# Kernel optimization log

Measured on AMD Instinct MI355X. Metric: run time of the kernel, lower is better.

## Reference

```python
import jax, jax.numpy as jnp
import numpy as np

B, T, D = 8, 1024, 1024
H = 16
DH = D // H  # 64


def setup_inputs() -> dict:
    key = jax.random.key(0)
    k1, k2, k3 = jax.random.split(key, 3)
    x = jax.random.normal(k1, (B, T, D), dtype=jnp.float32)
    W_qkv = jax.random.normal(k2, (3 * D, D), dtype=jnp.float32) * (D ** -0.5)
    W_proj = jax.random.normal(k3, (D, D), dtype=jnp.float32) * (D ** -0.5)
    return {"x": x, "W_qkv": W_qkv, "W_proj": W_proj}


def reference(x, W_qkv, W_proj):
    b, t, _ = x.shape
    # qkv: [B,T,3*D] -> [B,T,3,H,DH]
    qkv = (x @ W_qkv.T).reshape(b, t, 3, H, DH)
    q, k, v = qkv[:, :, 0], qkv[:, :, 1], qkv[:, :, 2]  # [B,T,H,DH]
    scale = DH ** -0.5
    # scores: [B,H,Tq,Tk]
    scores = jnp.einsum("bqhd,bkhd->bhqk", q, k) * scale
    # NOTE: softmax over dim=-2 (the QUERY axis), as in the original module
    attn = jax.nn.softmax(scores, axis=-2)
    out = jnp.einsum("bhqk,bkhd->bqhd", attn, v).reshape(b, t, D)
    return out @ W_proj.T
```

## Files before the change

### kernel.cpp

```cpp
#include <hip/hip_runtime.h>


typedef __bf16 bf16_t;
typedef __bf16 bf16x8 __attribute__((ext_vector_type(8)));
typedef __bf16 bf16x4 __attribute__((ext_vector_type(4)));
typedef float f32x4 __attribute__((ext_vector_type(4)));
typedef unsigned short u16x8 __attribute__((ext_vector_type(8)));

#define DEV __device__ __forceinline__
#define C2 0.18033688f

DEV void gld_lds16(const bf16_t* g, bf16_t* l) {
  __builtin_amdgcn_global_load_lds(
      (const __attribute__((address_space(1))) unsigned int*)g,
      (__attribute__((address_space(3))) unsigned int*)l, 16, 0, 0);
}

DEV float exp2c(float x) { return __builtin_amdgcn_exp2f(fminf(x, 30.f)); }
DEV float sanit(float v) { return (v == v) ? fminf(fmaxf(v, -1e4f), 1e4f) : 0.f; }

DEV int sw64(int r, int kc) { return r * 64 + (((kc ^ (r + (r >> 3))) & 7) << 3); }

DEV f32x4 mfma16(bf16x8 a, bf16x8 b, f32x4 c) {
  return __builtin_amdgcn_mfma_f32_16x16x32_bf16(a, b, c, 0, 0, 0);
}

__global__ void detect_dtype(const unsigned short* x, int* flag) {
  __shared__ int smax;
  if (threadIdx.x == 0) smax = 0;
  __syncthreads();
  int m = 0;
  for (int i = threadIdx.x; i < 16384; i += 256) {
    int e = (x[i] >> 7) & 0xFF;
    m = m > e ? m : e;
  }
  atomicMax(&smax, m);
  __syncthreads();
  if (threadIdx.x == 0) *flag = (smax >= 160) ? 1 : 0;
}

__global__ void convert_in(const void* __restrict__ x, const void* __restrict__ wq,
                           const void* __restrict__ wp, bf16_t* __restrict__ xb,
                           bf16_t* __restrict__ wqb, bf16_t* __restrict__ wpb,
                           const int* __restrict__ flag) {
  int i = blockIdx.x * 256 + threadIdx.x;
  const void* src;
  bf16_t* dst;
  int off;
  if (i < 1048576) { src = x; dst = xb; off = i; }
  else if (i < 1441792) { src = wq; dst = wqb; off = i - 1048576; }
  else { src = wp; dst = wpb; off = i - 1441792; }
  if (*flag) {
    const float4* s = (const float4*)src;
    float4 a = s[off * 2], b = s[off * 2 + 1];
    bf16x8 o;
    o[0] = (bf16_t)a.x; o[1] = (bf16_t)a.y; o[2] = (bf16_t)a.z; o[3] = (bf16_t)a.w;
    o[4] = (bf16_t)b.x; o[5] = (bf16_t)b.y; o[6] = (bf16_t)b.z; o[7] = (bf16_t)b.w;
    *(bf16x8*)(dst + (size_t)off * 8) = o;
  } else {
    ((u16x8*)dst)[off] = ((const u16x8*)src)[off];
  }
}

__global__ __launch_bounds__(256, 2)
void gemm_bt(const bf16_t* __restrict__ A, int lda, const bf16_t* __restrict__ B,
             bf16_t* __restrict__ Cb, float* __restrict__ Cf, int ldc,
             int K, const int* __restrict__ f32flag) {
  __shared__ bf16_t sA0[128 * 64];
  __shared__ bf16_t sB0[128 * 64];
  __shared__ bf16_t sA1[128 * 64];
  __shared__ bf16_t sB1[128 * 64];
  const int tid = threadIdx.x;
  const int wave = tid >> 6, lane = tid & 63;
  const int l = lane & 15, quad = lane >> 4;
  const int nwg = gridDim.x * gridDim.y;
  const int bid = blockIdx.y * gridDim.x + blockIdx.x;
  const int sb = (bid & 7) * (nwg >> 3) + (bid >> 3);
  const int row0 = (sb / gridDim.x) * 128, col0 = (sb % gridDim.x) * 128;
  const int wm = (wave >> 1) * 64, wn = (wave & 1) * 64;
  f32x4 acc[4][4];
#pragma unroll
  for (int i = 0; i < 4; ++i)
#pragma unroll
    for (int j = 0; j < 4; ++j) acc[i][j] = f32x4{0.f, 0.f, 0.f, 0.f};

#define STAGE_G(sa, sb_, kk)                                                  \
  {                                                                           \
    _Pragma("unroll") for (int t = 0; t < 4; ++t) {                           \
      int n = t * 256 + tid;                                                  \
      int r = n >> 3;                                                         \
      int kc = ((n & 7) ^ (r + (r >> 3))) & 7;                                \
      gld_lds16(A + (size_t)(row0 + r) * lda + (kk) + kc * 8, (sa) + n * 8);  \
      gld_lds16(B + (size_t)(col0 + r) * K + (kk) + kc * 8, (sb_) + n * 8);   \
    }                                                                         \
  }

#define COMPUTE_G(sa, sb_)                                                    \
  {                                                                           \
    _Pragma("unroll") for (int ks = 0; ks < 2; ++ks) {                        \
      bf16x8 af[4], bfr[4];                                                   \
      _Pragma("unroll") for (int i = 0; i < 4; ++i) af[i] =                   \
          *(const bf16x8*)&(sa)[sw64(wm + i * 16 + l, ks * 4 + quad)];        \
      _Pragma("unroll") for (int j = 0; j < 4; ++j) bfr[j] =                  \
          *(const bf16x8*)&(sb_)[sw64(wn + j * 16 + l, ks * 4 + quad)];       \
      _Pragma("unroll") for (int i = 0; i < 4; ++i)                           \
          _Pragma("unroll") for (int j = 0; j < 4; ++j) acc[i][j] =           \
              mfma16(af[i], bfr[j], acc[i][j]);                               \
    }                                                                         \
  }

  STAGE_G(sA0, sB0, 0);
  for (int k0 = 0; k0 < K; k0 += 128) {
    __syncthreads();
    if (k0 + 64 < K) STAGE_G(sA1, sB1, k0 + 64);
    COMPUTE_G(sA0, sB0);
    __syncthreads();
    if (k0 + 128 < K) STAGE_G(sA0, sB0, k0 + 128);
    COMPUTE_G(sA1, sB1);
  }
#undef STAGE_G
#undef COMPUTE_G

  const bool of32 = (f32flag != nullptr) && (*f32flag != 0);
#pragma unroll
  for (int i = 0; i < 4; ++i) {
    int rr = row0 + wm + i * 16 + quad * 4;
#pragma unroll
    for (int j = 0; j < 4; ++j) {
      int cc = col0 + wn + j * 16 + l;
#pragma unroll
      for (int t = 0; t < 4; ++t) {
        float v = sanit(acc[i][j][t]);
        size_t idx = (size_t)(rr + t) * ldc + cc;
        if (of32) Cf[idx] = v; else Cb[idx] = (bf16_t)v;
      }
    }
  }
}

__global__ __launch_bounds__(256, 4)
void attn_stats(const bf16_t* __restrict__ qkv, bf16_t* __restrict__ Vts) {
  __shared__ bf16_t sK[128 * 64];
  __shared__ bf16_t sV[128 * 64];
  __shared__ float sL[128];
  const int bh = blockIdx.x, kt = blockIdx.y;
  const int b = bh >> 4, h = bh & 15;
  const int tid = threadIdx.x, wave = tid >> 6, lane = tid & 63;
  const int l = lane & 15, quad = lane >> 4;
  const size_t rowK = (size_t)b * 1024 + kt * 128;

#pragma unroll
  for (int t = 0; t < 4; ++t) {
    int base = wave * 256 + t * 64;
    int n = base + lane;
    int r = n >> 3;
    int kc = ((n & 7) ^ (r + (r >> 3))) & 7;
    gld_lds16(qkv + (rowK + r) * 3072 + 2048 + h * 64 + kc * 8, sV + base * 8);
    gld_lds16(qkv + (rowK + r) * 3072 + 1024 + h * 64 + kc * 8, sK + base * 8);
  }
  if (tid < 128) sL[tid] = 0.f;
  __syncthreads();

  float accj[8];
#pragma unroll
  for (int j = 0; j < 8; ++j) accj[j] = 0.f;

  for (int qt = 0; qt < 8; ++qt) {
    bf16x8 aq[2][2];
#pragma unroll
    for (int i = 0; i < 2; ++i)
#pragma unroll
      for (int ks = 0; ks < 2; ++ks)
        aq[i][ks] = *(const bf16x8*)&qkv[((size_t)b * 1024 + qt * 128 + wave * 32 +
                                          i * 16 + l) * 3072 + h * 64 +
                                         (ks * 4 + quad) * 8];
#pragma unroll
    for (int j = 0; j < 8; ++j) {
      f32x4 s0 = {0.f, 0.f, 0.f, 0.f}, s1 = {0.f, 0.f, 0.f, 0.f};
#pragma unroll
      for (int ks = 0; ks < 2; ++ks) {
        bf16x8 bk = *(const bf16x8*)&sK[sw64(j * 16 + l, ks * 4 + quad)];
        s0 = mfma16(aq[0][ks], bk, s0);
        s1 = mfma16(aq[1][ks], bk, s1);
      }
#pragma unroll
      for (int t = 0; t < 4; ++t)
        accj[j] += exp2c(s0[t] * C2) + exp2c(s1[t] * C2);
    }
  }
#pragma unroll
  for (int j = 0; j < 8; ++j) {
    float v = accj[j];
    v += __shfl_xor(v, 16);
    v += __shfl_xor(v, 32);
    if (lane < 16) atomicAdd(&sL[j * 16 + l], v);
  }
  __syncthreads();
  if (tid < 128) sL[tid] = 1.0f / fmaxf(sL[tid], 1e-20f);
  __syncthreads();

#pragma unroll
  for (int t = 0; t < 4; ++t) {
    int u = t * 256 + tid;
    int d = u >> 4, k0 = (u & 15) * 8;
    bf16x8 pk;
#pragma unroll
    for (int i = 0; i < 8; ++i) {
      int kl = (k0 & ~31) | ((i >> 2) << 4) | (((k0 >> 3) & 3) << 2) | (i & 3);
      float v = (float)sV[sw64(kl, d >> 3) + (d & 7)];
      pk[i] = (bf16_t)(v * sL[kl]);
    }
    *(bf16x8*)&Vts[((size_t)bh * 64 + d) * 1024 + kt * 128 + k0] = pk;
  }
}

__global__ __launch_bounds__(512, 4)
void attn_out_k(const bf16_t* __restrict__ qkv, const bf16_t* __restrict__ Vts,
                bf16_t* __restrict__ attn) {
  __shared__ bf16_t sK[2][128 * 64];
  __shared__ bf16_t sV[2][64 * 128];
  const int bh = blockIdx.x, qt = blockIdx.y;
  const int b = bh >> 4, h = bh & 15;
  const int tid = threadIdx.x, wave = tid >> 6, lane = tid & 63;
  const int l = lane & 15, quad = lane >> 4;
  const bf16_t* qbase = qkv + (size_t)b * 3145728 + h * 64;
  const bf16_t* vbase = Vts + (size_t)bh * 65536;

  bf16x8 bq[2][2];
#pragma unroll
  for (int i = 0; i < 2; ++i)
#pragma unroll
    for (int ks = 0; ks < 2; ++ks)
      bq[i][ks] = *(const bf16x8*)&qbase[(size_t)(qt * 256 + wave * 32 + i * 16 + l) *
                                             3072 + ks * 32 + quad * 8];
  f32x4 o[2][4];
#pragma unroll
  for (int i = 0; i < 2; ++i)
#pragma unroll
    for (int jd = 0; jd < 4; ++jd) o[i][jd] = f32x4{0.f, 0.f, 0.f, 0.f};

#pragma unroll
  for (int t = 0; t < 2; ++t) {
    int n = t * 512 + tid;
    int r = n >> 3;
    int kc = ((n & 7) ^ (r + (r >> 3))) & 7;
    gld_lds16(qkv + ((size_t)b * 1024 + r) * 3072 + 1024 + h * 64 + kc * 8,
              sK[0] + n * 8);
    int d = n >> 4, s = n & 15;
    int c = s ^ (d & 7);
    gld_lds16(vbase + (size_t)d * 1024 + c * 8, sV[0] + n * 8);
  }

  for (int kt = 0; kt < 8; ++kt) {
    const int buf = kt & 1;
    __syncthreads();
    if (kt < 7) {
#pragma unroll
      for (int t = 0; t < 2; ++t) {
        int n = t * 512 + tid;
        int r = n >> 3;
        int kc = ((n & 7) ^ (r + (r >> 3))) & 7;
        gld_lds16(qkv + ((size_t)b * 1024 + (kt + 1) * 128 + r) * 3072 + 1024 +
                      h * 64 + kc * 8,
                  sK[buf ^ 1] + n * 8);
        int d = n >> 4, s = n & 15;
        int c = s ^ (d & 7);
        gld_lds16(vbase + (size_t)d * 1024 + (kt + 1) * 128 + c * 8,
                  sV[buf ^ 1] + n * 8);
      }
    }
    const bf16_t* sKb = sK[buf];
    const bf16_t* sVb = sV[buf];

#pragma unroll
    for (int ch = 0; ch < 4; ++ch) {
      bf16x8 ak[2][2];
#pragma unroll
      for (int kk = 0; kk < 2; ++kk)
#pragma unroll
        for (int ks = 0; ks < 2; ++ks)
          ak[kk][ks] = *(const bf16x8*)&sKb[sw64(ch * 32 + kk * 16 + l,
                                                 ks * 4 + quad)];
      bf16x8 va[4];
#pragma unroll
      for (int jd = 0; jd < 4; ++jd)
        va[jd] = *(const bf16x8*)&sVb[(jd * 16 + l) * 128 +
                                      (((ch * 4 + quad) ^ (l & 7)) << 3)];
#pragma unroll
      for (int i = 0; i < 2; ++i) {
        __builtin_amdgcn_s_setprio(1);
        f32x4 st0 = {0.f, 0.f, 0.f, 0.f}, st1 = {0.f, 0.f, 0.f, 0.f};
        st0 = mfma16(ak[0][0], bq[i][0], st0);
        st0 = mfma16(ak[0][1], bq[i][1], st0);
        st1 = mfma16(ak[1][0], bq[i][0], st1);
        st1 = mfma16(ak[1][1], bq[i][1], st1);
        bf16x8 pc;
#pragma unroll
        for (int t = 0; t < 4; ++t) {
          pc[t] = (bf16_t)exp2c(st0[t] * C2);
          pc[4 + t] = (bf16_t)exp2c(st1[t] * C2);
        }
#pragma unroll
        for (int jd = 0; jd < 4; ++jd)
          o[i][jd] = mfma16(va[jd], pc, o[i][jd]);
        __builtin_amdgcn_s_setprio(0);
      }
    }
  }
#pragma unroll
  for (int i = 0; i < 2; ++i) {
    size_t row = (size_t)b * 1024 + qt * 256 + wave * 32 + i * 16 + l;
#pragma unroll
    for (int jd = 0; jd < 4; ++jd) {
      bf16x4 pk;
#pragma unroll
      for (int t = 0; t < 4; ++t) pk[t] = (bf16_t)sanit(o[i][jd][t]);
      *(bf16x4*)&attn[row * 3072 + h * 64 + jd * 16 + quad * 4] = pk;
    }
  }
}

extern "C" void kernel_launch(void* const* d_in, const int* in_sizes, int n_in,
                              void* d_out, int out_size, void* d_ws, size_t ws_size,
                              hipStream_t stream) {
  (void)in_sizes; (void)n_in; (void)out_size; (void)ws_size;
  char* w = (char*)d_ws;
  bf16_t* qkv = (bf16_t*)w;
  bf16_t* xb = (bf16_t*)(w + 50331648);
  bf16_t* Vts = xb;
  bf16_t* Wqkvb = (bf16_t*)(w + 67108864);
  bf16_t* Wprojb = (bf16_t*)(w + 73400320);
  int* flag = (int*)(w + 75497472);
  bf16_t* attn = qkv + 2048;

  detect_dtype<<<1, 256, 0, stream>>>((const unsigned short*)d_in[0], flag);
  convert_in<<<6144, 256, 0, stream>>>(d_in[0], d_in[1], d_in[2],
                                       xb, Wqkvb, Wprojb, flag);

  gemm_bt<<<dim3(24, 64), 256, 0, stream>>>(xb, 1024, Wqkvb, qkv, nullptr, 3072,
                                            1024, nullptr);
  attn_stats<<<dim3(128, 8), 256, 0, stream>>>(qkv, Vts);
  attn_out_k<<<dim3(128, 4), 512, 0, stream>>>(qkv, Vts, attn);
  gemm_bt<<<dim3(8, 64), 256, 0, stream>>>(attn, 3072, Wprojb, (bf16_t*)d_out,
                                           (float*)d_out, 1024, 1024, flag);
}
```

Before: 266.4 us.

## Fold softmax scale into Q weights and double-buffer Q loads in colsum pass

Pre-multiplies the Q rows of W_qkv by the softmax scale times log2(e) during input conversion, so both attention passes skip the per-score multiply before exp2. The column-sum pass now loads Q fragments into two alternating register buffers so the next tile's global loads overlap the current tile's MFMAs and exponentials. It also raises wave priority around the QK MFMAs. Scaling the weights before the bf16 rounding changes rounding slightly, and the extra buffer raises register pressure.

```diff
diff --git a/kernel.cpp b/kernel.cpp
--- a/kernel.cpp
+++ b/kernel.cpp
@@ -47,18 +47,33 @@
   const void* src;
   bf16_t* dst;
   int off;
+  bool isQ = false;
   if (i < 1048576) { src = x; dst = xb; off = i; }
-  else if (i < 1441792) { src = wq; dst = wqb; off = i - 1048576; }
-  else { src = wp; dst = wpb; off = i - 1441792; }
+  else if (i < 1441792) {
+    src = wq; dst = wqb; off = i - 1048576;
+    isQ = off < 131072;
+  } else { src = wp; dst = wpb; off = i - 1441792; }
+  const float s = isQ ? C2 : 1.0f;
   if (*flag) {
-    const float4* s = (const float4*)src;
-    float4 a = s[off * 2], b = s[off * 2 + 1];
+    const float4* sp = (const float4*)src;
+    float4 a = sp[off * 2], b = sp[off * 2 + 1];
     bf16x8 o;
-    o[0] = (bf16_t)a.x; o[1] = (bf16_t)a.y; o[2] = (bf16_t)a.z; o[3] = (bf16_t)a.w;
-    o[4] = (bf16_t)b.x; o[5] = (bf16_t)b.y; o[6] = (bf16_t)b.z; o[7] = (bf16_t)b.w;
+    o[0] = (bf16_t)(a.x * s); o[1] = (bf16_t)(a.y * s);
+    o[2] = (bf16_t)(a.z * s); o[3] = (bf16_t)(a.w * s);
+    o[4] = (bf16_t)(b.x * s); o[5] = (bf16_t)(b.y * s);
+    o[6] = (bf16_t)(b.z * s); o[7] = (bf16_t)(b.w * s);
     *(bf16x8*)(dst + (size_t)off * 8) = o;
   } else {
-    ((u16x8*)dst)[off] = ((const u16x8*)src)[off];
+    u16x8 v = ((const u16x8*)src)[off];
+    if (isQ) {
+      bf16x8 bsrc = __builtin_bit_cast(bf16x8, v);
+      bf16x8 o;
+#pragma unroll
+      for (int t = 0; t < 8; ++t) o[t] = (bf16_t)((float)bsrc[t] * C2);
+      *(bf16x8*)(dst + (size_t)off * 8) = o;
+    } else {
+      ((u16x8*)dst)[off] = v;
+    }
   }
 }
 
@@ -165,29 +180,43 @@
 #pragma unroll
   for (int j = 0; j < 8; ++j) accj[j] = 0.f;
 
-  for (int qt = 0; qt < 8; ++qt) {
-    bf16x8 aq[2][2];
-#pragma unroll
-    for (int i = 0; i < 2; ++i)
-#pragma unroll
-      for (int ks = 0; ks < 2; ++ks)
-        aq[i][ks] = *(const bf16x8*)&qkv[((size_t)b * 1024 + qt * 128 + wave * 32 +
-                                          i * 16 + l) * 3072 + h * 64 +
-                                         (ks * 4 + quad) * 8];
-#pragma unroll
-    for (int j = 0; j < 8; ++j) {
-      f32x4 s0 = {0.f, 0.f, 0.f, 0.f}, s1 = {0.f, 0.f, 0.f, 0.f};
-#pragma unroll
-      for (int ks = 0; ks < 2; ++ks) {
-        bf16x8 bk = *(const bf16x8*)&sK[sw64(j * 16 + l, ks * 4 + quad)];
-        s0 = mfma16(aq[0][ks], bk, s0);
-        s1 = mfma16(aq[1][ks], bk, s1);
-      }
-#pragma unroll
-      for (int t = 0; t < 4; ++t)
-        accj[j] += exp2c(s0[t] * C2) + exp2c(s1[t] * C2);
-    }
-  }
+#define LOADQ(aq, qt)                                                         \
+  {                                                                           \
+    _Pragma("unroll") for (int i = 0; i < 2; ++i)                             \
+        _Pragma("unroll") for (int ks = 0; ks < 2; ++ks) (aq)[i][ks] =        \
+            *(const bf16x8*)&qkv[((size_t)b * 1024 + (qt) * 128 + wave * 32 + \
+                                  i * 16 + l) * 3072 + h * 64 +               \
+                                 (ks * 4 + quad) * 8];                        \
+  }
+
+#define QKBODY(aq)                                                            \
+  {                                                                           \
+    _Pragma("unroll") for (int j = 0; j < 8; ++j) {                           \
+      f32x4 s0 = {0.f, 0.f, 0.f, 0.f}, s1 = {0.f, 0.f, 0.f, 0.f};            \
+      __builtin_amdgcn_s_setprio(1);                                          \
+      _Pragma("unroll") for (int ks = 0; ks < 2; ++ks) {                      \
+        bf16x8 bk = *(const bf16x8*)&sK[sw64(j * 16 + l, ks * 4 + quad)];     \
+        s0 = mfma16((aq)[0][ks], bk, s0);                                     \
+        s1 = mfma16((aq)[1][ks], bk, s1);                                     \
+      }                                                                       \
+      __builtin_amdgcn_s_setprio(0);                                          \
+      _Pragma("unroll") for (int t = 0; t < 4; ++t) accj[j] +=                \
+          exp2c(s0[t]) + exp2c(s1[t]);                                        \
+    }                                                                         \
+  }
+
+  bf16x8 aqA[2][2], aqB[2][2];
+  LOADQ(aqA, 0);
+#pragma unroll
+  for (int qt = 0; qt < 8; qt += 2) {
+    LOADQ(aqB, qt + 1);
+    QKBODY(aqA);
+    if (qt + 2 < 8) LOADQ(aqA, qt + 2);
+    QKBODY(aqB);
+  }
+#undef LOADQ
+#undef QKBODY
+
 #pragma unroll
   for (int j = 0; j < 8; ++j) {
     float v = accj[j];
@@ -297,8 +326,8 @@
         bf16x8 pc;
 #pragma unroll
         for (int t = 0; t < 4; ++t) {
-          pc[t] = (bf16_t)exp2c(st0[t] * C2);
-          pc[4 + t] = (bf16_t)exp2c(st1[t] * C2);
+          pc[t] = (bf16_t)exp2c(st0[t]);
+          pc[4 + t] = (bf16_t)exp2c(st1[t]);
         }
 #pragma unroll
         for (int jd = 0; jd < 4; ++jd)
```

After: 426.5 us. 1.6x slower.
